# Kernel tuning notes

Measured on AMD Instinct MI355X. Metric: run time of the kernel, lower is better.

Reference implementation:

```python
import jax, jax.numpy as jnp
import numpy as np

B, Nq, C, H = 1, 300, 256, 8
h, w = 32, 32
HW = h * w
HID = 512  # rpe_hidden_dim
HD = C // H


def setup_inputs() -> dict:
    key = jax.random.key(0)
    ks = jax.random.split(key, 16)
    s = 0.02
    inp = {
        "raw_query": jax.random.normal(ks[0], (B, Nq, C), jnp.float32),
        "query_pos": jax.random.normal(ks[1], (B, Nq, C), jnp.float32),
        "reference_points": jax.random.uniform(ks[2], (B, Nq, 2), jnp.float32),
        "raw_src": jax.random.normal(ks[3], (B, HW, C), jnp.float32),
        "src_pos_embed": jax.random.normal(ks[4], (B, HW, C), jnp.float32),
        "Wq": jax.random.normal(ks[5], (C, C), jnp.float32) * s,
        "bq": jnp.zeros((C,), jnp.float32),
        "Wk": jax.random.normal(ks[6], (C, C), jnp.float32) * s,
        "bk": jnp.zeros((C,), jnp.float32),
        "Wv": jax.random.normal(ks[7], (C, C), jnp.float32) * s,
        "bv": jnp.zeros((C,), jnp.float32),
        "Wo": jax.random.normal(ks[8], (C, C), jnp.float32) * s,
        "bo": jnp.zeros((C,), jnp.float32),
        "W1": jax.random.normal(ks[9], (HID, 2), jnp.float32),   # cpb MLP layer 1
        "b1": jnp.zeros((HID,), jnp.float32),
        "W2": jax.random.normal(ks[10], (H, HID), jnp.float32) * s,  # cpb MLP layer 2 (no bias)
        "input_spatial_shapes": np.array([[h, w]], dtype=np.int64),
    }
    return inp


def _key_positions(hh, ww):
    ys = (jnp.arange(hh, dtype=jnp.float32) + 0.5) / hh
    xs = (jnp.arange(ww, dtype=jnp.float32) + 0.5) / ww
    yy, xx = jnp.meshgrid(ys, xs, indexing="ij")  # row-major: idx = y*w + x
    return jnp.stack([xx.ravel(), yy.ravel()], axis=-1)  # [HW, 2] (x, y)


def reference(raw_query, query_pos, reference_points, raw_src, src_pos_embed,
              Wq, bq, Wk, bk, Wv, bv, Wo, bo, W1, b1, W2, input_spatial_shapes):
    hh, ww = int(input_spatial_shapes[0, 0]), int(input_spatial_shapes[0, 1])
    scale = HD ** (-0.5)
    queries = raw_query + query_pos                      # [B,Nq,C]
    memory = raw_src + src_pos_embed                     # [B,HW,C]

    q = (queries @ Wq.T + bq).reshape(B, Nq, H, HD)
    k = (memory @ Wk.T + bk).reshape(B, hh * ww, H, HD)
    v = (memory @ Wv.T + bv).reshape(B, hh * ww, H, HD)

    logits = jnp.einsum("bqhd,bkhd->bhqk", q, k) * scale  # [B,H,Nq,HW]

    key_pos = _key_positions(hh, ww)                      # [HW,2]
    delta = reference_points[:, :, None, :] - key_pos[None, None]  # [B,Nq,HW,2]
    hid = jax.nn.relu(jnp.einsum("bqkc,hc->bqkh", delta, W1) + b1)  # [B,Nq,HW,HID]
    bias = jnp.einsum("bqkf,hf->bhqk", hid, W2)           # [B,H,Nq,HW]

    attn = jax.nn.softmax(logits + bias, axis=-1)
    out = jnp.einsum("bhqk,bkhd->bqhd", attn, v).reshape(B, Nq, C)
    return out @ Wo.T + bo
```

## Files before the change

kernel.cpp:

```cpp
#include <hip/hip_runtime.h>
#include <hip/hip_fp16.h>
#include <stdint.h>

#define NQ   300
#define CDIM 256
#define NH   8
#define HD   32
#define HWK  1024
#define HIDD 512

typedef __attribute__((ext_vector_type(8))) _Float16 f16x8;
typedef __attribute__((ext_vector_type(2))) _Float16 h2v;
typedef __attribute__((ext_vector_type(4))) float f32x4;

#define QB_OFF   0
#define KB_OFF   153600
#define VT_OFF   677888
#define PO_OFF   1202176
#define PL_OFF   3659776
#define A16_OFF  3736576
#define NX_OFF   4043776
#define NY_OFF   4044800
#define W2_OFF   4045824

__device__ __forceinline__ short f16b(float x){
  _Float16 h = (_Float16)x;
  return __builtin_bit_cast(short, h);
}

__device__ __forceinline__ uint32_t pk_f16(float a, float b){
  auto r = __builtin_amdgcn_cvt_pkrtz(a, b);
  return __builtin_bit_cast(uint32_t, r);
}

__global__ __launch_bounds__(256) void proj_kernel(
    const float* __restrict__ rq, const float* __restrict__ qp,
    const float* __restrict__ rs, const float* __restrict__ spe,
    const float* __restrict__ Wq, const float* __restrict__ bq,
    const float* __restrict__ Wk, const float* __restrict__ bk,
    const float* __restrict__ Wv, const float* __restrict__ bv,
    const float* __restrict__ refp, const float* __restrict__ W1,
    const float* __restrict__ b1, const float* __restrict__ W2,
    char* __restrict__ ws)
{
  int bxid = blockIdx.x;
  __shared__ __align__(16) float At[32][20];
  __shared__ float Wl[32][129];

  if (bxid >= 294){
    int idx = (bxid - 294) * 256 + threadIdx.x;
    short* a16  = (short*)(ws + A16_OFF);
    short* nx16 = (short*)(ws + NX_OFF);
    short* ny16 = (short*)(ws + NY_OFF);
    short* w216 = (short*)(ws + W2_OFF);
    if (idx < NQ*HIDD){
      int q = idx >> 9, f = idx & 511;
      float2 w = ((const float2*)W1)[f];
      float a = fmaf(w.x, refp[2*q], fmaf(w.y, refp[2*q+1], b1[f]));
      a16[idx] = f16b(a);
    } else {
      int j = idx - NQ*HIDD;
      if (j < HIDD){
        float2 w = ((const float2*)W1)[j];
        nx16[j] = f16b(-w.x);
        ny16[j] = f16b(-w.y);
      } else if (j < HIDD + NH*HIDD){
        int e = j - HIDD;
        w216[e] = f16b(W2[e]);
      }
    }
    return;
  }

  int tile = bxid >> 1, half = bxid & 1;
  const float *in1, *in2, *W, *bias;
  int r0, M, mode;
  if (tile < 19){
    in1 = rq; in2 = qp; W = Wq; bias = bq; r0 = tile*16; M = NQ; mode = 0;
  } else if (tile < 83){
    in1 = rs; in2 = spe; W = Wk; bias = bk; r0 = (tile-19)*16; M = HWK; mode = 1;
  } else {
    in1 = rs; in2 = spe; W = Wv; bias = bv; r0 = (tile-83)*16; M = HWK; mode = 2;
  }
  int tid = threadIdx.x;
  int n_loc = tid & 127;
  int rg = tid >> 7;
  int n = half*128 + n_loc;
  float acc[8];
  float bv_ = bias[n];
  #pragma unroll
  for (int i=0;i<8;i++) acc[i] = bv_;

  for (int c0 = 0; c0 < CDIM; c0 += 32){
    __syncthreads();
    for (int e = tid; e < 512; e += 256){
      int r = e >> 5, c = e & 31;
      int gr = r0 + r; if (gr >= M) gr = M - 1;
      At[c][r] = in1[gr*CDIM + c0 + c] + in2[gr*CDIM + c0 + c];
    }
    for (int e = tid; e < 4096; e += 256){
      int c = e & 31, nn = e >> 5;
      Wl[c][nn] = W[(half*128 + nn)*CDIM + c0 + c];
    }
    __syncthreads();
    #pragma unroll
    for (int c = 0; c < 32; c++){
      float w = Wl[c][n_loc];
      const float4* ap = (const float4*)&At[c][rg*8];
      float4 a0 = ap[0], a1 = ap[1];
      acc[0] = fmaf(a0.x, w, acc[0]);
      acc[1] = fmaf(a0.y, w, acc[1]);
      acc[2] = fmaf(a0.z, w, acc[2]);
      acc[3] = fmaf(a0.w, w, acc[3]);
      acc[4] = fmaf(a1.x, w, acc[4]);
      acc[5] = fmaf(a1.y, w, acc[5]);
      acc[6] = fmaf(a1.z, w, acc[6]);
      acc[7] = fmaf(a1.w, w, acc[7]);
    }
  }

  if (mode == 0){
    short* qb = (short*)(ws + QB_OFF);
    const float s = 0.17677669529663687f;
    #pragma unroll
    for (int i=0;i<8;i++){
      int gr = r0 + rg*8 + i;
      if (gr < M) qb[gr*CDIM + n] = f16b(acc[i]*s);
    }
  } else if (mode == 1){
    short* kb = (short*)(ws + KB_OFF);
    int h = n >> 5, d = n & 31;
    #pragma unroll
    for (int i=0;i<8;i++){
      int gr = r0 + rg*8 + i;
      if (gr < M) kb[((size_t)h*HWK + gr)*HD + d] = f16b(acc[i]);
    }
  } else {
    short* vt = (short*)(ws + VT_OFF);
    uint32_t p[4];
    #pragma unroll
    for (int i=0;i<4;i++) p[i] = pk_f16(acc[2*i], acc[2*i+1]);
    *(uint4*)(vt + n*HWK + r0 + rg*8) = make_uint4(p[0], p[1], p[2], p[3]);
  }
}

__global__ __launch_bounds__(256, 4) void fused_kernel(
    const short* __restrict__ a16, const short* __restrict__ nx16,
    const short* __restrict__ ny16, const short* __restrict__ w216,
    const short* __restrict__ qb, const short* __restrict__ kb,
    const short* __restrict__ vt, float* __restrict__ po,
    float* __restrict__ pl)
{
  int bid = blockIdx.x;
  int q0 = (bid >> 3) * 2, kr = bid & 7;
  int tid = threadIdx.x, wave = tid >> 6, lane = tid & 63;
  int n = lane & 15, qd = lane >> 4;

  __shared__ __align__(16) _Float16 nwx[HIDD];
  __shared__ __align__(16) char pool[8192];
  __shared__ __align__(16) _Float16 w2l[NH][520];
  __shared__ __align__(16) _Float16 pb[2][NH][136];
  __shared__ float lsum[4][16];
  _Float16 (*c1s)[4][HIDD] = (_Float16 (*)[4][HIDD])pool;
  float (*part)[4][NH][32] = (float (*)[4][NH][32])pool;

  {
    int f0 = tid * 2;
    h2v ny2 = *(const h2v*)(ny16 + f0);
    h2v nx2 = *(const h2v*)(nx16 + f0);
    *(h2v*)&nwx[f0] = nx2;
    #pragma unroll
    for (int qq = 0; qq < 2; qq++){
      h2v a2 = *(const h2v*)(a16 + (q0+qq)*HIDD + f0);
      #pragma unroll
      for (int r = 0; r < 4; r++){
        _Float16 kyh = (_Float16)(((float)(kr*4 + r) + 0.5f) * (1.0f/32.0f));
        h2v ky2 = {kyh, kyh};
        *(h2v*)&c1s[qq][r][f0] = ny2 * ky2 + a2;
      }
    }
  }
  for (int e = tid; e < 512; e += 256){
    int r = e >> 6, c = e & 63;
    *(f16x8*)&w2l[r][c*8] = *(const f16x8*)(w216 + r*HIDD + c*8);
  }
  f16x8 qfrag = *(const f16x8*)(qb + (q0 + (n >> 3))*CDIM + (n & 7)*HD + qd*8);
  f16x8 qm[NH];
  #pragma unroll
  for (int h = 0; h < NH; h++){
    f16x8 z = {0,0,0,0,0,0,0,0};
    qm[h] = ((n & 7) == h) ? qfrag : z;
  }
  __syncthreads();

  const int kyrow = kr*4 + wave;
  const int kbase = kyrow * 32;

  f32x4 acc1[2] = {{0.f,0.f,0.f,0.f},{0.f,0.f,0.f,0.f}};
  #pragma unroll
  for (int t = 0; t < 2; t++){
    int k0 = kbase + t*16;
    #pragma unroll
    for (int h = 0; h < NH; h++){
      f16x8 af = *(const f16x8*)(kb + ((size_t)h*HWK + k0 + n)*HD + qd*8);
      acc1[t] = __builtin_amdgcn_mfma_f32_16x16x32_f16(af, qm[h], acc1[t], 0, 0, 0);
    }
  }

  _Float16 kxAh = (_Float16)(((float)n + 0.5f) * (1.0f/32.0f));
  _Float16 kxBh = (_Float16)(((float)n + 16.5f) * (1.0f/32.0f));
  f16x8 kxA8, kxB8, z8;
  #pragma unroll
  for (int j = 0; j < 8; j++){ kxA8[j] = kxAh; kxB8[j] = kxBh; z8[j] = (_Float16)0.f; }
  f32x4 accb[2][2];
  accb[0][0] = acc1[0]; accb[0][1] = acc1[1];
  accb[1][0] = acc1[0]; accb[1][1] = acc1[1];
  const _Float16* c1r0 = &c1s[0][wave][0];
  const _Float16* c1r1 = &c1s[1][wave][0];
  #pragma unroll 4
  for (int kc = 0; kc < 16; kc++){
    int f0 = kc*32 + qd*8;
    f16x8 c10 = *(const f16x8*)(c1r0 + f0);
    f16x8 c11 = *(const f16x8*)(c1r1 + f0);
    f16x8 wxv = *(const f16x8*)(&nwx[f0]);
    f16x8 bfr = *(const f16x8*)(&w2l[n & 7][f0]);
    #pragma unroll
    for (int t = 0; t < 2; t++){
      f16x8 kx8 = t ? kxB8 : kxA8;
      f16x8 e0 = __builtin_elementwise_max(wxv * kx8 + c10, z8);
      accb[0][t] = __builtin_amdgcn_mfma_f32_16x16x32_f16(e0, bfr, accb[0][t], 0, 0, 0);
      f16x8 e1 = __builtin_elementwise_max(wxv * kx8 + c11, z8);
      accb[1][t] = __builtin_amdgcn_mfma_f32_16x16x32_f16(e1, bfr, accb[1][t], 0, 0, 0);
    }
  }

  int qsel = n >> 3, hsel = n & 7;
  float lacc = 0.f;
  #pragma unroll
  for (int t = 0; t < 2; t++){
    f32x4 a = qsel ? accb[1][t] : accb[0][t];
    float e0 = __expf(a[0]);
    float e1 = __expf(a[1]);
    float e2 = __expf(a[2]);
    float e3 = __expf(a[3]);
    uint2 p2;
    p2.x = pk_f16(e0, e1);
    p2.y = pk_f16(e2, e3);
    *(uint2*)&pb[qsel][hsel][wave*32 + t*16 + qd*4] = p2;
    float s = e0 + e1 + e2 + e3;
    s += __shfl_xor(s, 16);
    s += __shfl_xor(s, 32);
    lacc += s;
  }
  if (lane < 16) lsum[wave][lane] = lacc;

  #pragma unroll
  for (int h = 0; h < NH; h++){
    int kl = wave*32 + qd*8;
    f16x8 pa = *(const f16x8*)&pb[n & 1][h][kl];
    f16x8 v0 = *(const f16x8*)(vt + ((size_t)(h*HD +      n))*HWK + kr*128 + kl);
    f16x8 v1 = *(const f16x8*)(vt + ((size_t)(h*HD + 16 + n))*HWK + kr*128 + kl);
    f32x4 o0 = {0.f,0.f,0.f,0.f}, o1 = {0.f,0.f,0.f,0.f};
    o0 = __builtin_amdgcn_mfma_f32_16x16x32_f16(pa, v0, o0, 0, 0, 0);
    o1 = __builtin_amdgcn_mfma_f32_16x16x32_f16(pa, v1, o1, 0, 0, 0);
    if (qd == 0){
      part[0][wave][h][n]      = o0[0];
      part[1][wave][h][n]      = o0[1];
      part[0][wave][h][16 + n] = o1[0];
      part[1][wave][h][16 + n] = o1[1];
    }
  }
  __syncthreads();

  {
    int h = tid >> 5, d = tid & 31;
    #pragma unroll
    for (int qq = 0; qq < 2; qq++){
      float s = part[qq][0][h][d] + part[qq][1][h][d]
              + part[qq][2][h][d] + part[qq][3][h][d];
      po[((size_t)kr*NQ + q0 + qq)*CDIM + tid] = s;
    }
    if (tid < 16){
      float s = lsum[0][tid] + lsum[1][tid] + lsum[2][tid] + lsum[3][tid];
      pl[((size_t)kr*NQ + q0 + (tid >> 3))*NH + (tid & 7)] = s;
    }
  }
}

__global__ __launch_bounds__(256) void outproj_kernel(
    const float* __restrict__ po, const float* __restrict__ pl,
    const float* __restrict__ Wo, const float* __restrict__ bo,
    float* __restrict__ dout)
{
  int q = blockIdx.x;
  int tid = threadIdx.x;
  __shared__ __align__(16) float a_lds[CDIM];
  __shared__ float linv[NH];

  float s = 0.f;
  #pragma unroll
  for (int p = 0; p < 8; p++) s += po[((size_t)p*NQ + q)*CDIM + tid];

  if (tid < 64){
    int p = tid >> 3, h = tid & 7;
    float l = pl[((size_t)p*NQ + q)*NH + h];
    l += __shfl_xor(l, 8);
    l += __shfl_xor(l, 16);
    l += __shfl_xor(l, 32);
    if (p == 0) linv[h] = 1.0f / l;
  }
  __syncthreads();
  a_lds[tid] = s * linv[tid >> 5];
  __syncthreads();

  const float4* wrow = (const float4*)(Wo + (size_t)tid*CDIM);
  const float4* av = (const float4*)a_lds;
  float acc0 = bo[tid], acc1 = 0.f, acc2 = 0.f, acc3 = 0.f;
  #pragma unroll 4
  for (int c = 0; c < 64; c += 4){
    float4 w0 = wrow[c+0], a0 = av[c+0];
    float4 w1 = wrow[c+1], a1 = av[c+1];
    float4 w2 = wrow[c+2], a2 = av[c+2];
    float4 w3 = wrow[c+3], a3 = av[c+3];
    acc0 = fmaf(w0.x,a0.x,fmaf(w0.y,a0.y,fmaf(w0.z,a0.z,fmaf(w0.w,a0.w,acc0))));
    acc1 = fmaf(w1.x,a1.x,fmaf(w1.y,a1.y,fmaf(w1.z,a1.z,fmaf(w1.w,a1.w,acc1))));
    acc2 = fmaf(w2.x,a2.x,fmaf(w2.y,a2.y,fmaf(w2.z,a2.z,fmaf(w2.w,a2.w,acc2))));
    acc3 = fmaf(w3.x,a3.x,fmaf(w3.y,a3.y,fmaf(w3.z,a3.z,fmaf(w3.w,a3.w,acc3))));
  }
  dout[(size_t)q*CDIM + tid] = acc0 + acc1 + acc2 + acc3;
}

extern "C" void kernel_launch(void* const* d_in, const int* in_sizes, int n_in,
                              void* d_out, int out_size, void* d_ws, size_t ws_size,
                              hipStream_t stream)
{
  const float* rq  = (const float*)d_in[0];
  const float* qp  = (const float*)d_in[1];
  const float* rp  = (const float*)d_in[2];
  const float* rs  = (const float*)d_in[3];
  const float* spe = (const float*)d_in[4];
  const float* Wq  = (const float*)d_in[5];
  const float* bq  = (const float*)d_in[6];
  const float* Wk  = (const float*)d_in[7];
  const float* bk  = (const float*)d_in[8];
  const float* Wv  = (const float*)d_in[9];
  const float* bv  = (const float*)d_in[10];
  const float* Wo  = (const float*)d_in[11];
  const float* bo  = (const float*)d_in[12];
  const float* W1  = (const float*)d_in[13];
  const float* b1  = (const float*)d_in[14];
  const float* W2  = (const float*)d_in[15];
  char* ws = (char*)d_ws;
  float* dout = (float*)d_out;

  proj_kernel<<<912, 256, 0, stream>>>(rq, qp, rs, spe, Wq, bq, Wk, bk,
      Wv, bv, rp, W1, b1, W2, ws);
  fused_kernel<<<1200, 256, 0, stream>>>((const short*)(ws + A16_OFF),
      (const short*)(ws + NX_OFF), (const short*)(ws + NY_OFF),
      (const short*)(ws + W2_OFF), (const short*)(ws + QB_OFF),
      (const short*)(ws + KB_OFF), (const short*)(ws + VT_OFF),
      (float*)(ws + PO_OFF), (float*)(ws + PL_OFF));
  outproj_kernel<<<300, 256, 0, stream>>>((const float*)(ws + PO_OFF),
      (const float*)(ws + PL_OFF), Wo, bo, dout);
}
```

Before: 144.3 us.

## Split key range into 16 chunks per query pair to double fused grid

The fused attention kernel now splits the 1024 keys into 16 chunks of 64 instead of 8 chunks of 128, launching 2400 blocks. Each wave handles one 16-key tile instead of two, and the PV stage is reorganised so waves split key halves and output-dim halves. The occupancy hint rises from 4 to 6 blocks per CU. The partial-output buffers move to a larger workspace region, and outproj now reduces 16 partials instead of 8. The goal is more parallelism and fewer registers per thread, at the cost of duplicated per-block setup, an extra barrier, and twice as much partial-sum traffic.

```diff
diff --git a/kernel.cpp b/kernel.cpp
--- a/kernel.cpp
+++ b/kernel.cpp
@@ -16,12 +16,12 @@
 #define QB_OFF   0
 #define KB_OFF   153600
 #define VT_OFF   677888
-#define PO_OFF   1202176
-#define PL_OFF   3659776
 #define A16_OFF  3736576
 #define NX_OFF   4043776
 #define NY_OFF   4044800
 #define W2_OFF   4045824
+#define PO_OFF   4200448
+#define PL_OFF   9120000
 
 __device__ __forceinline__ short f16b(float x){
   _Float16 h = (_Float16)x;
@@ -144,7 +144,7 @@
   }
 }
 
-__global__ __launch_bounds__(256, 4) void fused_kernel(
+__global__ __launch_bounds__(256, 6) void fused_kernel(
     const short* __restrict__ a16, const short* __restrict__ nx16,
     const short* __restrict__ ny16, const short* __restrict__ w216,
     const short* __restrict__ qb, const short* __restrict__ kb,
@@ -152,17 +152,17 @@
     float* __restrict__ pl)
 {
   int bid = blockIdx.x;
-  int q0 = (bid >> 3) * 2, kr = bid & 7;
+  int q0 = (bid >> 4) * 2, kr = bid & 15;
   int tid = threadIdx.x, wave = tid >> 6, lane = tid & 63;
   int n = lane & 15, qd = lane >> 4;
+  int r = wave & 1, th = wave >> 1;
 
   __shared__ __align__(16) _Float16 nwx[HIDD];
-  __shared__ __align__(16) char pool[8192];
+  __shared__ __align__(16) _Float16 c1s[2][2][HIDD];
   __shared__ __align__(16) _Float16 w2l[NH][520];
-  __shared__ __align__(16) _Float16 pb[2][NH][136];
+  __shared__ __align__(16) _Float16 pb[2][NH][72];
+  __shared__ __align__(16) float part[2][4][NH][16];
   __shared__ float lsum[4][16];
-  _Float16 (*c1s)[4][HIDD] = (_Float16 (*)[4][HIDD])pool;
-  float (*part)[4][NH][32] = (float (*)[4][NH][32])pool;
 
   {
     int f0 = tid * 2;
@@ -173,16 +173,16 @@
     for (int qq = 0; qq < 2; qq++){
       h2v a2 = *(const h2v*)(a16 + (q0+qq)*HIDD + f0);
       #pragma unroll
-      for (int r = 0; r < 4; r++){
-        _Float16 kyh = (_Float16)(((float)(kr*4 + r) + 0.5f) * (1.0f/32.0f));
+      for (int rr = 0; rr < 2; rr++){
+        _Float16 kyh = (_Float16)(((float)(kr*2 + rr) + 0.5f) * (1.0f/32.0f));
         h2v ky2 = {kyh, kyh};
-        *(h2v*)&c1s[qq][r][f0] = ny2 * ky2 + a2;
+        *(h2v*)&c1s[qq][rr][f0] = ny2 * ky2 + a2;
       }
     }
   }
   for (int e = tid; e < 512; e += 256){
-    int r = e >> 6, c = e & 63;
-    *(f16x8*)&w2l[r][c*8] = *(const f16x8*)(w216 + r*HIDD + c*8);
+    int rw = e >> 6, c = e & 63;
+    *(f16x8*)&w2l[rw][c*8] = *(const f16x8*)(w216 + rw*HIDD + c*8);
   }
   f16x8 qfrag = *(const f16x8*)(qb + (q0 + (n >> 3))*CDIM + (n & 7)*HD + qd*8);
   f16x8 qm[NH];
@@ -193,52 +193,41 @@
   }
   __syncthreads();
 
-  const int kyrow = kr*4 + wave;
-  const int kbase = kyrow * 32;
-
-  f32x4 acc1[2] = {{0.f,0.f,0.f,0.f},{0.f,0.f,0.f,0.f}};
-  #pragma unroll
-  for (int t = 0; t < 2; t++){
-    int k0 = kbase + t*16;
-    #pragma unroll
-    for (int h = 0; h < NH; h++){
-      f16x8 af = *(const f16x8*)(kb + ((size_t)h*HWK + k0 + n)*HD + qd*8);
-      acc1[t] = __builtin_amdgcn_mfma_f32_16x16x32_f16(af, qm[h], acc1[t], 0, 0, 0);
-    }
-  }
-
-  _Float16 kxAh = (_Float16)(((float)n + 0.5f) * (1.0f/32.0f));
-  _Float16 kxBh = (_Float16)(((float)n + 16.5f) * (1.0f/32.0f));
-  f16x8 kxA8, kxB8, z8;
-  #pragma unroll
-  for (int j = 0; j < 8; j++){ kxA8[j] = kxAh; kxB8[j] = kxBh; z8[j] = (_Float16)0.f; }
-  f32x4 accb[2][2];
-  accb[0][0] = acc1[0]; accb[0][1] = acc1[1];
-  accb[1][0] = acc1[0]; accb[1][1] = acc1[1];
-  const _Float16* c1r0 = &c1s[0][wave][0];
-  const _Float16* c1r1 = &c1s[1][wave][0];
+  const int kyrow = kr*2 + r;
+  const int k0 = kyrow*32 + th*16;
+
+  f32x4 acc1 = {0.f,0.f,0.f,0.f};
+  #pragma unroll
+  for (int h = 0; h < NH; h++){
+    f16x8 af = *(const f16x8*)(kb + ((size_t)h*HWK + k0 + n)*HD + qd*8);
+    acc1 = __builtin_amdgcn_mfma_f32_16x16x32_f16(af, qm[h], acc1, 0, 0, 0);
+  }
+
+  _Float16 kxh = (_Float16)(((float)(th*16 + n) + 0.5f) * (1.0f/32.0f));
+  f16x8 kx8, z8;
+  #pragma unroll
+  for (int j = 0; j < 8; j++){ kx8[j] = kxh; z8[j] = (_Float16)0.f; }
+  f32x4 accb[2];
+  accb[0] = acc1; accb[1] = acc1;
+  const _Float16* c1r0 = &c1s[0][r][0];
+  const _Float16* c1r1 = &c1s[1][r][0];
   #pragma unroll 4
   for (int kc = 0; kc < 16; kc++){
-    int f0 = kc*32 + qd*8;
-    f16x8 c10 = *(const f16x8*)(c1r0 + f0);
-    f16x8 c11 = *(const f16x8*)(c1r1 + f0);
-    f16x8 wxv = *(const f16x8*)(&nwx[f0]);
-    f16x8 bfr = *(const f16x8*)(&w2l[n & 7][f0]);
-    #pragma unroll
-    for (int t = 0; t < 2; t++){
-      f16x8 kx8 = t ? kxB8 : kxA8;
-      f16x8 e0 = __builtin_elementwise_max(wxv * kx8 + c10, z8);
-      accb[0][t] = __builtin_amdgcn_mfma_f32_16x16x32_f16(e0, bfr, accb[0][t], 0, 0, 0);
-      f16x8 e1 = __builtin_elementwise_max(wxv * kx8 + c11, z8);
-      accb[1][t] = __builtin_amdgcn_mfma_f32_16x16x32_f16(e1, bfr, accb[1][t], 0, 0, 0);
-    }
+    int ff = kc*32 + qd*8;
+    f16x8 c10 = *(const f16x8*)(c1r0 + ff);
+    f16x8 c11 = *(const f16x8*)(c1r1 + ff);
+    f16x8 wxv = *(const f16x8*)(&nwx[ff]);
+    f16x8 bfr = *(const f16x8*)(&w2l[n & 7][ff]);
+    f16x8 e0 = __builtin_elementwise_max(wxv * kx8 + c10, z8);
+    accb[0] = __builtin_amdgcn_mfma_f32_16x16x32_f16(e0, bfr, accb[0], 0, 0, 0);
+    f16x8 e1 = __builtin_elementwise_max(wxv * kx8 + c11, z8);
+    accb[1] = __builtin_amdgcn_mfma_f32_16x16x32_f16(e1, bfr, accb[1], 0, 0, 0);
   }
 
   int qsel = n >> 3, hsel = n & 7;
-  float lacc = 0.f;
-  #pragma unroll
-  for (int t = 0; t < 2; t++){
-    f32x4 a = qsel ? accb[1][t] : accb[0][t];
+  float lacc;
+  {
+    f32x4 a = qsel ? accb[1] : accb[0];
     float e0 = __expf(a[0]);
     float e1 = __expf(a[1]);
     float e2 = __expf(a[2]);
@@ -246,38 +235,37 @@
     uint2 p2;
     p2.x = pk_f16(e0, e1);
     p2.y = pk_f16(e2, e3);
-    *(uint2*)&pb[qsel][hsel][wave*32 + t*16 + qd*4] = p2;
+    *(uint2*)&pb[qsel][hsel][r*32 + th*16 + qd*4] = p2;
     float s = e0 + e1 + e2 + e3;
     s += __shfl_xor(s, 16);
     s += __shfl_xor(s, 32);
-    lacc += s;
+    lacc = s;
   }
   if (lane < 16) lsum[wave][lane] = lacc;
-
-  #pragma unroll
-  for (int h = 0; h < NH; h++){
-    int kl = wave*32 + qd*8;
-    f16x8 pa = *(const f16x8*)&pb[n & 1][h][kl];
-    f16x8 v0 = *(const f16x8*)(vt + ((size_t)(h*HD +      n))*HWK + kr*128 + kl);
-    f16x8 v1 = *(const f16x8*)(vt + ((size_t)(h*HD + 16 + n))*HWK + kr*128 + kl);
-    f32x4 o0 = {0.f,0.f,0.f,0.f}, o1 = {0.f,0.f,0.f,0.f};
-    o0 = __builtin_amdgcn_mfma_f32_16x16x32_f16(pa, v0, o0, 0, 0, 0);
-    o1 = __builtin_amdgcn_mfma_f32_16x16x32_f16(pa, v1, o1, 0, 0, 0);
-    if (qd == 0){
-      part[0][wave][h][n]      = o0[0];
-      part[1][wave][h][n]      = o0[1];
-      part[0][wave][h][16 + n] = o1[0];
-      part[1][wave][h][16 + n] = o1[1];
+  __syncthreads();
+
+  {
+    int c = wave & 1, oh = wave >> 1;
+    #pragma unroll
+    for (int h = 0; h < NH; h++){
+      f16x8 pa = *(const f16x8*)&pb[n & 1][h][c*32 + qd*8];
+      f16x8 v0 = *(const f16x8*)(vt + ((size_t)(h*HD + oh*16 + n))*HWK + kr*64 + c*32 + qd*8);
+      f32x4 o0 = {0.f,0.f,0.f,0.f};
+      o0 = __builtin_amdgcn_mfma_f32_16x16x32_f16(pa, v0, o0, 0, 0, 0);
+      if (qd == 0){
+        part[0][wave][h][n] = o0[0];
+        part[1][wave][h][n] = o0[1];
+      }
     }
   }
   __syncthreads();
 
   {
     int h = tid >> 5, d = tid & 31;
+    int oh = d >> 4, dn = d & 15;
     #pragma unroll
     for (int qq = 0; qq < 2; qq++){
-      float s = part[qq][0][h][d] + part[qq][1][h][d]
-              + part[qq][2][h][d] + part[qq][3][h][d];
+      float s = part[qq][oh*2 + 0][h][dn] + part[qq][oh*2 + 1][h][dn];
       po[((size_t)kr*NQ + q0 + qq)*CDIM + tid] = s;
     }
     if (tid < 16){
@@ -299,11 +287,12 @@
 
   float s = 0.f;
   #pragma unroll
-  for (int p = 0; p < 8; p++) s += po[((size_t)p*NQ + q)*CDIM + tid];
+  for (int p = 0; p < 16; p++) s += po[((size_t)p*NQ + q)*CDIM + tid];
 
   if (tid < 64){
     int p = tid >> 3, h = tid & 7;
-    float l = pl[((size_t)p*NQ + q)*NH + h];
+    float l = pl[((size_t)p*NQ + q)*NH + h]
+            + pl[((size_t)(p+8)*NQ + q)*NH + h];
     l += __shfl_xor(l, 8);
     l += __shfl_xor(l, 16);
     l += __shfl_xor(l, 32);
@@ -355,7 +344,7 @@
 
   proj_kernel<<<912, 256, 0, stream>>>(rq, qp, rs, spe, Wq, bq, Wk, bk,
       Wv, bv, rp, W1, b1, W2, ws);
-  fused_kernel<<<1200, 256, 0, stream>>>((const short*)(ws + A16_OFF),
+  fused_kernel<<<2400, 256, 0, stream>>>((const short*)(ws + A16_OFF),
       (const short*)(ws + NX_OFF), (const short*)(ws + NY_OFF),
       (const short*)(ws + W2_OFF), (const short*)(ws + QB_OFF),
       (const short*)(ws + KB_OFF), (const short*)(ws + VT_OFF),
```

Result: no change. 144.6 us (+0.1%).
